# Performance work log

Measured on AMD Instinct MI355X. Metric: run time of the kernel, lower is better.

The kernel has to match this reference:

```python
import jax, jax.numpy as jnp
import numpy as np

# ---- static config (matches init_kwargs) ----
OC, IC, K, S, PAD = 128, 64, 3, 1, 1
M, T, R = 5, 8, 2.5            # ALSH m, table_size, LSH bucket width r
SPAN = K * K * IC              # kernel_span = 576


def setup_inputs() -> dict:
    key = jax.random.key(0)
    k1, k2, k3, k4 = jax.random.split(key, 4)
    # xavier_uniform on the (OC, SPAN) kernel matrix
    bound = float(np.sqrt(6.0 / (OC + SPAN)))
    kernels = jax.random.uniform(k1, (OC, SPAN), minval=-bound, maxval=bound, dtype=jnp.float32)
    a = jax.random.normal(k2, (SPAN + M,), dtype=jnp.float32)          # LSH projection
    b = jax.random.uniform(k3, (), minval=0.0, maxval=R, dtype=jnp.float32)  # LSH offset
    x = jax.random.normal(k4, (16, IC, 56, 56), dtype=jnp.float32)
    return {"x": x, "kernels": kernels, "a": a, "b": b, "mode": 0}


def _im2col(x):
    # [B, SPAN, H2, W2] with feature order (C, kh, kw)
    p = jax.lax.conv_general_dilated_patches(x, (K, K), (S, S), [(PAD, PAD), (PAD, PAD)])
    B, _, H2, W2 = p.shape
    # patch matrix [SPAN, B*H2*W2]
    return p.transpose(1, 0, 2, 3).reshape(SPAN, -1), B, H2, W2


def _bucket(h):
    # floor((h+b)/r); fmod table_size; abs  (matches torch .fmod_ then .abs_)
    return jnp.abs(jnp.fmod(h.astype(jnp.int32), T))


def reference(x, kernels, a, b, mode):
    patch_matr, B, H2, W2 = _im2col(x)            # [SPAN, N], N = B*H2*W2

    # ---- vote: hash every patch column with Q-augmentation (append m halves) ----
    v = a[:SPAN] @ patch_matr + 0.5 * jnp.sum(a[SPAN:])      # [N]
    votes = _bucket(jnp.floor((v + b) / R))
    counts = jnp.zeros((T,), jnp.int32).at[votes].add(1)
    bucket = jnp.argmax(counts)                               # most common bucket

    # ---- hash table: hash each kernel row with P-augmentation (norm powers) ----
    norms2 = jnp.sum(kernels * kernels, axis=1)               # ||k||^2, [OC]
    powers = jnp.stack([norms2 ** (2 ** i) for i in range(M)], axis=1)  # ||k||^{2,4,...,2^M}
    hk = kernels @ a[:SPAN] + powers @ a[SPAN:]               # [OC]
    kidx = _bucket(jnp.floor((hk + b) / R))                   # bucket of each kernel

    # ---- select kernels in the winning bucket; scale by |rows|/OC ----
    mask = (kidx == bucket).astype(x.dtype)                   # [OC]
    cnt = jnp.sum(mask)
    # original gathers the selected rows (variable oc); we scatter back to the
    # full OC channels (zeros for inactive kernels) for static shapes.
    # empty bucket -> dense conv with all kernels, no rescale.
    factor = jnp.where(cnt > 0, mask * (OC / jnp.maximum(cnt, 1.0)), jnp.ones_like(mask))

    out = (kernels * factor[:, None]) @ patch_matr            # [OC, N]
    out = out.reshape(OC, B, H2 * W2).transpose(1, 0, 2)
    return out.reshape(B, OC, H2, W2)
```

## Files before the change

### kernel.cpp

```cpp
#include <hip/hip_runtime.h>
#include <math.h>

#define IC 64
#define OC 128
#define HH 56
#define WW 56
#define BATCH 16
#define HP 58
#define HW (HH*WW)
#define NPIX (BATCH*HW)
#define SPAN 576
#define TSIZE 8
#define VBANDS 28
#define VBLOCKS (BATCH*VBANDS)
#define W2BASE  VBLOCKS
#define BORDBASE (VBLOCKS + OC)
#define NBLK1 (BORDBASE + BATCH)

typedef unsigned short ushort_t;
typedef unsigned int uint_t;
typedef __attribute__((ext_vector_type(8))) __bf16 bf16x8;
typedef __attribute__((ext_vector_type(4))) float f32x4;

__device__ __forceinline__ ushort_t bf16_rne(float f) {
  uint_t u = __builtin_bit_cast(uint_t, f);
  u += 0x7FFFu + ((u >> 16) & 1u);
  return (ushort_t)(u >> 16);
}

__global__ __launch_bounds__(256)
void prep_kernel(const float* __restrict__ x, const float* __restrict__ kernels,
                 const float* __restrict__ a, const float* __restrict__ bptr,
                 ushort_t* __restrict__ xpad, ushort_t* __restrict__ w2,
                 int* __restrict__ rbucket, int* __restrict__ hist_partial) {
  __shared__ float tl[224 * 9];
  __shared__ ushort_t lx[112 * 66];
  __shared__ int hist[TSIZE];
  __shared__ float red0[256], red1[256];
  const int bx = blockIdx.x, t = threadIdx.x;

  if (bx < VBLOCKS) {
    const int b = bx / VBANDS, band = bx % VBANDS;
    const int r0 = band * 2;
    if (t < TSIZE) hist[t] = 0;
    if (t < 224) {
      const int prow = r0 - 1 + t / 56;
      const int col = t % 56;
      const bool inr = ((unsigned)prow < (unsigned)HH);
      const bool mid = (t >= 56 && t < 168);
      const float* xb = x + (size_t)b * IC * HW + (inr ? prow * WW + col : 0);
      ushort_t* lxp = lx + (mid ? (t - 56) : 0) * 66;
      float t9[9] = {0, 0, 0, 0, 0, 0, 0, 0, 0};
      #pragma unroll 8
      for (int c = 0; c < IC; ++c) {
        float xv = inr ? xb[(size_t)c * HW] : 0.0f;
        #pragma unroll
        for (int tap = 0; tap < 9; ++tap) t9[tap] += a[c * 9 + tap] * xv;
        if (mid) lxp[c] = bf16_rne(xv);
      }
      #pragma unroll
      for (int tap = 0; tap < 9; ++tap) tl[t * 9 + tap] = t9[tap];
    }
    __syncthreads();
    if (t < 112) {
      int lr = t / 56, col = t % 56;
      float v = 0.0f;
      #pragma unroll
      for (int kh = 0; kh < 3; ++kh) {
        int gr = r0 + lr - 1 + kh;
        #pragma unroll
        for (int kw = 0; kw < 3; ++kw) {
          int cc = col - 1 + kw;
          if ((unsigned)gr < (unsigned)HH && (unsigned)cc < (unsigned)WW)
            v += tl[((lr + kh) * 56 + cc) * 9 + (kh * 3 + kw)];
        }
      }
      float tail = 0.5f * (a[576] + a[577] + a[578] + a[579] + a[580]);
      int hi = (int)floorf((v + tail + bptr[0]) / 2.5f);
      int r = hi % TSIZE;
      if (r < 0) r = -r;
      atomicAdd(&hist[r], 1);
    }
    {
      const uint_t* lxu = (const uint_t*)lx;
      uint_t* xp = (uint_t*)xpad;
      #pragma unroll
      for (int j = 0; j < 14; ++j) {
        int idx = j * 256 + t;
        int px = idx >> 5, cp = idx & 31;
        int lr = px / 56, c0 = px % 56;
        int y = r0 + 1 + lr, xw = c0 + 1;
        xp[(((size_t)(b * HP + y)) * HP + xw) * 32 + cp] = lxu[px * 33 + cp];
      }
    }
    __syncthreads();
    if (t < TSIZE) hist_partial[bx * TSIZE + t] = hist[t];
  } else if (bx < BORDBASE) {
    const int r = bx - W2BASE;
    const float* row = kernels + (size_t)r * SPAN;
    float d = 0.0f, n2 = 0.0f;
    #pragma unroll
    for (int k0 = 0; k0 < 3; ++k0) {
      int k = k0 * 256 + t;
      if (k < SPAN) { float kv = row[k]; d += kv * a[k]; n2 += kv * kv; }
    }
    red0[t] = d; red1[t] = n2;
    __syncthreads();
    for (int s = 128; s > 0; s >>= 1) {
      if (t < s) { red0[t] += red0[t + s]; red1[t] += red1[t + s]; }
      __syncthreads();
    }
    if (t == 0) {
      float hk = red0[0], p = red1[0];
      #pragma unroll
      for (int i = 0; i < 5; ++i) { hk += p * a[SPAN + i]; p = p * p; }
      int hi = (int)floorf((hk + bptr[0]) / 2.5f);
      int rr = hi % TSIZE;
      if (rr < 0) rr = -rr;
      rbucket[r] = rr;
    }
    #pragma unroll
    for (int j0 = 0; j0 < 3; ++j0) {
      int j = j0 * 256 + t;
      if (j < SPAN) {
        int tap = j >> 6, c = j & 63;
        w2[(size_t)r * SPAN + j] = bf16_rne(row[c * 9 + tap]);
      }
    }
  } else {
    const int ib = bx - BORDBASE;
    uint_t* xp = (uint_t*)xpad + (size_t)ib * HP * HP * 32;
    for (int j = t; j < 7296; j += 256) {
      int px = j >> 5, cp = j & 31;
      int y, xw;
      if (px < 58) { y = 0; xw = px; }
      else if (px < 116) { y = 57; xw = px - 58; }
      else { int k = px - 116; y = 1 + (k >> 1); xw = (k & 1) * 57; }
      xp[((size_t)y * HP + xw) * 32 + cp] = 0;
    }
  }
}

__global__ __launch_bounds__(256, 4)
void gemm_kernel(const ushort_t* __restrict__ w2, const ushort_t* __restrict__ xpad,
                 const int* __restrict__ hist_partial, const int* __restrict__ rbucket,
                 float* __restrict__ out) {
  __shared__ ushort_t As[128 * 64];
  __shared__ ushort_t Bs[64 * 64];
  __shared__ float factor_s[OC];
  __shared__ int counts_s[TSIZE];
  __shared__ int cnt_w[4];
  const int tid = threadIdx.x;
  const int wave = tid >> 6, lane = tid & 63;
  const int n0 = blockIdx.x * 64;
  const int wm = wave * 32;

  const int srow = lane >> 3;
  const int sch = (lane & 7) ^ srow;

  int agbase[4], bgbase[2];
  #pragma unroll
  for (int i = 0; i < 4; ++i) {
    int row = wm + i * 8 + srow;
    agbase[i] = row * SPAN + sch * 8;
  }
  #pragma unroll
  for (int i = 0; i < 2; ++i) {
    int brow = wave * 16 + i * 8 + srow;
    int n = n0 + brow;
    int b = n / HW;
    int rem = n % HW;
    int h = rem / WW, w = rem % WW;
    bgbase[i] = ((b * HP + h) * HP + w) * IC + sch * 8;
  }

  f32x4 acc[2][4] = {};

  for (int tap = 0; tap < 9; ++tap) {
    const int kh = tap / 3, kw = tap % 3;
    const int toffA = tap * 64;
    const int toffB = (kh * HP + kw) * IC;
    __syncthreads();
    #pragma unroll
    for (int i = 0; i < 4; ++i)
      __builtin_amdgcn_global_load_lds(
          (const __attribute__((address_space(1))) void*)(w2 + agbase[i] + toffA),
          (__attribute__((address_space(3))) void*)(As + (wm + i * 8) * 64), 16, 0, 0);
    #pragma unroll
    for (int i = 0; i < 2; ++i)
      __builtin_amdgcn_global_load_lds(
          (const __attribute__((address_space(1))) void*)(xpad + bgbase[i] + toffB),
          (__attribute__((address_space(3))) void*)(Bs + (wave * 16 + i * 8) * 64), 16, 0, 0);
    __syncthreads();
    #pragma unroll
    for (int kk = 0; kk < 2; ++kk) {
      const int jf = kk * 4 + (lane >> 4);
      bf16x8 af[2], bfr[4];
      #pragma unroll
      for (int m = 0; m < 2; ++m) {
        int row = wm + m * 16 + (lane & 15);
        int slot = row * 8 + (jf ^ (row & 7));
        af[m] = *(const bf16x8*)(As + slot * 8);
      }
      #pragma unroll
      for (int n = 0; n < 4; ++n) {
        int col = n * 16 + (lane & 15);
        int slot = col * 8 + (jf ^ (col & 7));
        bfr[n] = *(const bf16x8*)(Bs + slot * 8);
      }
      #pragma unroll
      for (int m = 0; m < 2; ++m)
        #pragma unroll
        for (int n = 0; n < 4; ++n)
          acc[m][n] = __builtin_amdgcn_mfma_f32_16x16x32_bf16(af[m], bfr[n], acc[m][n], 0, 0, 0);
    }
  }

  if (tid < TSIZE) counts_s[tid] = 0;
  __syncthreads();
  {
    int bin = tid >> 5;
    int s = 0;
    for (int k = (tid & 31); k < VBLOCKS; k += 32) s += hist_partial[k * TSIZE + bin];
    atomicAdd(&counts_s[bin], s);
  }
  __syncthreads();
  int best = counts_s[0], bi = 0;
  #pragma unroll
  for (int i = 1; i < TSIZE; ++i) { int c = counts_s[i]; if (c > best) { best = c; bi = i; } }
  int isin = (tid < OC) ? ((rbucket[tid] == bi) ? 1 : 0) : 0;
  unsigned long long bal = __ballot(isin != 0);
  if (lane == 0) cnt_w[wave] = __popcll(bal);
  __syncthreads();
  int cnt = cnt_w[0] + cnt_w[1] + cnt_w[2] + cnt_w[3];
  if (tid < OC)
    factor_s[tid] = (cnt > 0) ? (isin ? 128.0f / (float)cnt : 0.0f) : 1.0f;
  __syncthreads();

  #pragma unroll
  for (int n = 0; n < 4; ++n) {
    int np = n0 + n * 16 + (lane & 15);
    int b = np / HW;
    int rem = np % HW;
    float* obase = out + ((size_t)b * OC) * HW + rem;
    #pragma unroll
    for (int m = 0; m < 2; ++m) {
      int ocb = wm + m * 16 + (lane >> 4) * 4;
      #pragma unroll
      for (int r = 0; r < 4; ++r) {
        obase[(size_t)(ocb + r) * HW] = acc[m][n][r] * factor_s[ocb + r];
      }
    }
  }
}

extern "C" void kernel_launch(void* const* d_in, const int* in_sizes, int n_in,
                              void* d_out, int out_size, void* d_ws, size_t ws_size,
                              hipStream_t stream) {
  (void)in_sizes; (void)n_in; (void)out_size; (void)ws_size;
  const float* x = (const float*)d_in[0];
  const float* kernels = (const float*)d_in[1];
  const float* a = (const float*)d_in[2];
  const float* b = (const float*)d_in[3];
  float* out = (float*)d_out;

  char* ws = (char*)d_ws;
  int* rbucket = (int*)ws;
  int* hist_partial = (int*)(ws + 512);
  ushort_t* w2 = (ushort_t*)(ws + 16384);
  ushort_t* xpad = (ushort_t*)(ws + 16384 + 147456);

  prep_kernel<<<NBLK1, 256, 0, stream>>>(x, kernels, a, b, xpad, w2, rbucket, hist_partial);
  gemm_kernel<<<NPIX / 64, 256, 0, stream>>>(w2, xpad, hist_partial, rbucket, out);
}
```

Baseline: 112.3 us.

## Fuse prep and GEMM kernels into one persistent launch with grid barrier

Result: slower. 402.1 us (+257.9%).

```diff
diff --git a/kernel.cpp b/kernel.cpp
--- a/kernel.cpp
+++ b/kernel.cpp
@@ -15,7 +15,8 @@
 #define VBLOCKS (BATCH*VBANDS)
 #define W2BASE  VBLOCKS
 #define BORDBASE (VBLOCKS + OC)
-#define NBLK1 (BORDBASE + BATCH)
+#define NBLK (NPIX/64)
+#define MAGIC 0x13579BDF
 
 typedef unsigned short ushort_t;
 typedef unsigned int uint_t;
@@ -28,28 +29,46 @@
   return (ushort_t)(u >> 16);
 }
 
-__global__ __launch_bounds__(256)
-void prep_kernel(const float* __restrict__ x, const float* __restrict__ kernels,
-                 const float* __restrict__ a, const float* __restrict__ bptr,
-                 ushort_t* __restrict__ xpad, ushort_t* __restrict__ w2,
-                 int* __restrict__ rbucket, int* __restrict__ hist_partial) {
-  __shared__ float tl[224 * 9];
-  __shared__ ushort_t lx[112 * 66];
-  __shared__ int hist[TSIZE];
-  __shared__ float red0[256], red1[256];
-  const int bx = blockIdx.x, t = threadIdx.x;
+union SMem {
+  struct {
+    ushort_t As[128 * 64];
+    ushort_t Bs[64 * 64];
+    float factor[OC];
+    int counts[TSIZE];
+    int cnt_w[4];
+  } g;
+  struct {
+    float tl[224 * 9];
+    ushort_t lx[112 * 66];
+    int hist[TSIZE];
+  } v;
+  struct {
+    float red0[256];
+    float red1[256];
+  } w;
+};
+
+__global__ __launch_bounds__(256, 4)
+void fused_kernel(const float* __restrict__ x, const float* __restrict__ kernels,
+                  const float* __restrict__ a, const float* __restrict__ bptr,
+                  ushort_t* __restrict__ xpad, ushort_t* __restrict__ w2,
+                  int* __restrict__ rbucket, int* __restrict__ hist_partial,
+                  int* __restrict__ bar, float* __restrict__ out) {
+  __shared__ SMem sm;
+  const int bx = blockIdx.x;
+  const int t = threadIdx.x;
 
   if (bx < VBLOCKS) {
     const int b = bx / VBANDS, band = bx % VBANDS;
     const int r0 = band * 2;
-    if (t < TSIZE) hist[t] = 0;
+    if (t < TSIZE) sm.v.hist[t] = 0;
     if (t < 224) {
       const int prow = r0 - 1 + t / 56;
       const int col = t % 56;
       const bool inr = ((unsigned)prow < (unsigned)HH);
       const bool mid = (t >= 56 && t < 168);
       const float* xb = x + (size_t)b * IC * HW + (inr ? prow * WW + col : 0);
-      ushort_t* lxp = lx + (mid ? (t - 56) : 0) * 66;
+      ushort_t* lxp = sm.v.lx + (mid ? (t - 56) : 0) * 66;
       float t9[9] = {0, 0, 0, 0, 0, 0, 0, 0, 0};
       #pragma unroll 8
       for (int c = 0; c < IC; ++c) {
@@ -59,7 +78,7 @@
         if (mid) lxp[c] = bf16_rne(xv);
       }
       #pragma unroll
-      for (int tap = 0; tap < 9; ++tap) tl[t * 9 + tap] = t9[tap];
+      for (int tap = 0; tap < 9; ++tap) sm.v.tl[t * 9 + tap] = t9[tap];
     }
     __syncthreads();
     if (t < 112) {
@@ -72,17 +91,17 @@
         for (int kw = 0; kw < 3; ++kw) {
           int cc = col - 1 + kw;
           if ((unsigned)gr < (unsigned)HH && (unsigned)cc < (unsigned)WW)
-            v += tl[((lr + kh) * 56 + cc) * 9 + (kh * 3 + kw)];
+            v += sm.v.tl[((lr + kh) * 56 + cc) * 9 + (kh * 3 + kw)];
         }
       }
       float tail = 0.5f * (a[576] + a[577] + a[578] + a[579] + a[580]);
       int hi = (int)floorf((v + tail + bptr[0]) / 2.5f);
       int r = hi % TSIZE;
       if (r < 0) r = -r;
-      atomicAdd(&hist[r], 1);
+      atomicAdd(&sm.v.hist[r], 1);
     }
     {
-      const uint_t* lxu = (const uint_t*)lx;
+      const uint_t* lxu = (const uint_t*)sm.v.lx;
       uint_t* xp = (uint_t*)xpad;
       #pragma unroll
       for (int j = 0; j < 14; ++j) {
@@ -94,7 +113,7 @@
       }
     }
     __syncthreads();
-    if (t < TSIZE) hist_partial[bx * TSIZE + t] = hist[t];
+    if (t < TSIZE) hist_partial[bx * TSIZE + t] = sm.v.hist[t];
   } else if (bx < BORDBASE) {
     const int r = bx - W2BASE;
     const float* row = kernels + (size_t)r * SPAN;
@@ -104,14 +123,14 @@
       int k = k0 * 256 + t;
       if (k < SPAN) { float kv = row[k]; d += kv * a[k]; n2 += kv * kv; }
     }
-    red0[t] = d; red1[t] = n2;
+    sm.w.red0[t] = d; sm.w.red1[t] = n2;
     __syncthreads();
     for (int s = 128; s > 0; s >>= 1) {
-      if (t < s) { red0[t] += red0[t + s]; red1[t] += red1[t + s]; }
+      if (t < s) { sm.w.red0[t] += sm.w.red0[t + s]; sm.w.red1[t] += sm.w.red1[t + s]; }
       __syncthreads();
     }
     if (t == 0) {
-      float hk = red0[0], p = red1[0];
+      float hk = sm.w.red0[0], p = sm.w.red1[0];
       #pragma unroll
       for (int i = 0; i < 5; ++i) { hk += p * a[SPAN + i]; p = p * p; }
       int hi = (int)floorf((hk + bptr[0]) / 2.5f);
@@ -127,7 +146,7 @@
         w2[(size_t)r * SPAN + j] = bf16_rne(row[c * 9 + tap]);
       }
     }
-  } else {
+  } else if (bx < BORDBASE + BATCH) {
     const int ib = bx - BORDBASE;
     uint_t* xp = (uint_t*)xpad + (size_t)ib * HP * HP * 32;
     for (int j = t; j < 7296; j += 256) {
@@ -139,20 +158,35 @@
       xp[((size_t)y * HP + xw) * 32 + cp] = 0;
     }
   }
-}
-
-__global__ __launch_bounds__(256, 4)
-void gemm_kernel(const ushort_t* __restrict__ w2, const ushort_t* __restrict__ xpad,
-                 const int* __restrict__ hist_partial, const int* __restrict__ rbucket,
-                 float* __restrict__ out) {
-  __shared__ ushort_t As[128 * 64];
-  __shared__ ushort_t Bs[64 * 64];
-  __shared__ float factor_s[OC];
-  __shared__ int counts_s[TSIZE];
-  __shared__ int cnt_w[4];
-  const int tid = threadIdx.x;
-  const int wave = tid >> 6, lane = tid & 63;
-  const int n0 = blockIdx.x * 64;
+
+  __syncthreads();
+  if (t == 0) {
+    if (bx == 0) {
+      #pragma unroll
+      for (int i = 0; i < 8; ++i)
+        __hip_atomic_store(&bar[16 + i * 16], 0, __ATOMIC_RELAXED, __HIP_MEMORY_SCOPE_AGENT);
+      __hip_atomic_store(&bar[0], MAGIC, __ATOMIC_RELEASE, __HIP_MEMORY_SCOPE_AGENT);
+    } else {
+      int it = 0;
+      while (__hip_atomic_load(&bar[0], __ATOMIC_ACQUIRE, __HIP_MEMORY_SCOPE_AGENT) != MAGIC
+             && ++it < (1 << 26))
+        __builtin_amdgcn_s_sleep(2);
+    }
+    __hip_atomic_fetch_add(&bar[16 + (bx & 7) * 16], 1, __ATOMIC_ACQ_REL, __HIP_MEMORY_SCOPE_AGENT);
+    int it = 0;
+    for (;;) {
+      int sum = 0;
+      #pragma unroll
+      for (int i = 0; i < 8; ++i)
+        sum += __hip_atomic_load(&bar[16 + i * 16], __ATOMIC_ACQUIRE, __HIP_MEMORY_SCOPE_AGENT);
+      if (sum >= NBLK || ++it >= (1 << 26)) break;
+      __builtin_amdgcn_s_sleep(2);
+    }
+  }
+  __syncthreads();
+
+  const int wave = t >> 6, lane = t & 63;
+  const int n0 = bx * 64;
   const int wm = wave * 32;
 
   const int srow = lane >> 3;
@@ -185,12 +219,12 @@
     for (int i = 0; i < 4; ++i)
       __builtin_amdgcn_global_load_lds(
           (const __attribute__((address_space(1))) void*)(w2 + agbase[i] + toffA),
-          (__attribute__((address_space(3))) void*)(As + (wm + i * 8) * 64), 16, 0, 0);
+          (__attribute__((address_space(3))) void*)(sm.g.As + (wm + i * 8) * 64), 16, 0, 0);
     #pragma unroll
     for (int i = 0; i < 2; ++i)
       __builtin_amdgcn_global_load_lds(
           (const __attribute__((address_space(1))) void*)(xpad + bgbase[i] + toffB),
-          (__attribute__((address_space(3))) void*)(Bs + (wave * 16 + i * 8) * 64), 16, 0, 0);
+          (__attribute__((address_space(3))) void*)(sm.g.Bs + (wave * 16 + i * 8) * 64), 16, 0, 0);
     __syncthreads();
     #pragma unroll
     for (int kk = 0; kk < 2; ++kk) {
@@ -200,13 +234,13 @@
       for (int m = 0; m < 2; ++m) {
         int row = wm + m * 16 + (lane & 15);
         int slot = row * 8 + (jf ^ (row & 7));
-        af[m] = *(const bf16x8*)(As + slot * 8);
+        af[m] = *(const bf16x8*)(sm.g.As + slot * 8);
       }
       #pragma unroll
       for (int n = 0; n < 4; ++n) {
         int col = n * 16 + (lane & 15);
         int slot = col * 8 + (jf ^ (col & 7));
-        bfr[n] = *(const bf16x8*)(Bs + slot * 8);
+        bfr[n] = *(const bf16x8*)(sm.g.Bs + slot * 8);
       }
       #pragma unroll
       for (int m = 0; m < 2; ++m)
@@ -216,25 +250,25 @@
     }
   }
 
-  if (tid < TSIZE) counts_s[tid] = 0;
+  if (t < TSIZE) sm.g.counts[t] = 0;
   __syncthreads();
   {
-    int bin = tid >> 5;
+    int bin = t >> 5;
     int s = 0;
-    for (int k = (tid & 31); k < VBLOCKS; k += 32) s += hist_partial[k * TSIZE + bin];
-    atomicAdd(&counts_s[bin], s);
-  }
-  __syncthreads();
-  int best = counts_s[0], bi = 0;
+    for (int k = (t & 31); k < VBLOCKS; k += 32) s += hist_partial[k * TSIZE + bin];
+    atomicAdd(&sm.g.counts[bin], s);
+  }
+  __syncthreads();
+  int best = sm.g.counts[0], bi = 0;
   #pragma unroll
-  for (int i = 1; i < TSIZE; ++i) { int c = counts_s[i]; if (c > best) { best = c; bi = i; } }
-  int isin = (tid < OC) ? ((rbucket[tid] == bi) ? 1 : 0) : 0;
+  for (int i = 1; i < TSIZE; ++i) { int c = sm.g.counts[i]; if (c > best) { best = c; bi = i; } }
+  int isin = (t < OC) ? ((rbucket[t] == bi) ? 1 : 0) : 0;
   unsigned long long bal = __ballot(isin != 0);
-  if (lane == 0) cnt_w[wave] = __popcll(bal);
-  __syncthreads();
-  int cnt = cnt_w[0] + cnt_w[1] + cnt_w[2] + cnt_w[3];
-  if (tid < OC)
-    factor_s[tid] = (cnt > 0) ? (isin ? 128.0f / (float)cnt : 0.0f) : 1.0f;
+  if (lane == 0) sm.g.cnt_w[wave] = __popcll(bal);
+  __syncthreads();
+  int cnt = sm.g.cnt_w[0] + sm.g.cnt_w[1] + sm.g.cnt_w[2] + sm.g.cnt_w[3];
+  if (t < OC)
+    sm.g.factor[t] = (cnt > 0) ? (isin ? 128.0f / (float)cnt : 0.0f) : 1.0f;
   __syncthreads();
 
   #pragma unroll
@@ -248,7 +282,7 @@
       int ocb = wm + m * 16 + (lane >> 4) * 4;
       #pragma unroll
       for (int r = 0; r < 4; ++r) {
-        obase[(size_t)(ocb + r) * HW] = acc[m][n][r] * factor_s[ocb + r];
+        obase[(size_t)(ocb + r) * HW] = acc[m][n][r] * sm.g.factor[ocb + r];
       }
     }
   }
@@ -267,9 +301,10 @@
   char* ws = (char*)d_ws;
   int* rbucket = (int*)ws;
   int* hist_partial = (int*)(ws + 512);
+  int* bar = (int*)(ws + 15360);
   ushort_t* w2 = (ushort_t*)(ws + 16384);
   ushort_t* xpad = (ushort_t*)(ws + 16384 + 147456);
 
-  prep_kernel<<<NBLK1, 256, 0, stream>>>(x, kernels, a, b, xpad, w2, rbucket, hist_partial);
-  gemm_kernel<<<NPIX / 64, 256, 0, stream>>>(w2, xpad, hist_partial, rbucket, out);
+  fused_kernel<<<NBLK, 256, 0, stream>>>(x, kernels, a, b, xpad, w2,
+                                         rbucket, hist_partial, bar, out);
 }
```

## Pre-swizzle weights into MFMA fragment order for contiguous LDS reads

Applied to the files above, without the earlier changes.

After: 116.0 us. +3.3%, slower.

```diff
diff --git a/kernel.cpp b/kernel.cpp
--- a/kernel.cpp
+++ b/kernel.cpp
@@ -31,7 +31,7 @@
 __global__ __launch_bounds__(256)
 void prep_kernel(const float* __restrict__ x, const float* __restrict__ kernels,
                  const float* __restrict__ a, const float* __restrict__ bptr,
-                 ushort_t* __restrict__ xpad, ushort_t* __restrict__ w2,
+                 ushort_t* __restrict__ xpad, ushort_t* __restrict__ w2m,
                  int* __restrict__ rbucket, int* __restrict__ hist_partial) {
   __shared__ float tl[224 * 9];
   __shared__ ushort_t lx[112 * 66];
@@ -123,8 +123,10 @@
     for (int j0 = 0; j0 < 3; ++j0) {
       int j = j0 * 256 + t;
       if (j < SPAN) {
-        int tap = j >> 6, c = j & 63;
-        w2[(size_t)r * SPAN + j] = bf16_rne(row[c * 9 + tap]);
+        int tap = j / 64, rem = j % 64;
+        int chunk = rem >> 3, c = rem & 7;
+        w2m[(size_t)tap * 8192 + (r >> 4) * 1024 + chunk * 128 + (r & 15) * 8 + c] =
+            bf16_rne(row[rem * 9 + tap]);
       }
     }
   } else {
@@ -142,72 +144,58 @@
 }
 
 __global__ __launch_bounds__(256, 4)
-void gemm_kernel(const ushort_t* __restrict__ w2, const ushort_t* __restrict__ xpad,
+void gemm_kernel(const ushort_t* __restrict__ w2m, const ushort_t* __restrict__ xpad,
                  const int* __restrict__ hist_partial, const int* __restrict__ rbucket,
                  float* __restrict__ out) {
-  __shared__ ushort_t As[128 * 64];
-  __shared__ ushort_t Bs[64 * 64];
+  __shared__ ushort_t As[8192];
+  __shared__ ushort_t Bs[4096];
   __shared__ float factor_s[OC];
   __shared__ int counts_s[TSIZE];
   __shared__ int cnt_w[4];
   const int tid = threadIdx.x;
   const int wave = tid >> 6, lane = tid & 63;
   const int n0 = blockIdx.x * 64;
-  const int wm = wave * 32;
-
-  const int srow = lane >> 3;
-  const int sch = (lane & 7) ^ srow;
-
-  int agbase[4], bgbase[2];
+
+  int aseg[4];
   #pragma unroll
-  for (int i = 0; i < 4; ++i) {
-    int row = wm + i * 8 + srow;
-    agbase[i] = row * SPAN + sch * 8;
-  }
-  #pragma unroll
-  for (int i = 0; i < 2; ++i) {
-    int brow = wave * 16 + i * 8 + srow;
-    int n = n0 + brow;
-    int b = n / HW;
-    int rem = n % HW;
+  for (int i = 0; i < 4; ++i) aseg[i] = (wave * 4 + i) * 512 + lane * 8;
+
+  int bg;
+  {
+    int p = n0 + wave * 16 + (lane & 15);
+    int b = p / HW, rem = p % HW;
     int h = rem / WW, w = rem % WW;
-    bgbase[i] = ((b * HP + h) * HP + w) * IC + sch * 8;
+    bg = ((b * HP + h) * HP + w) * IC + (lane >> 4) * 8;
   }
 
   f32x4 acc[2][4] = {};
 
   for (int tap = 0; tap < 9; ++tap) {
     const int kh = tap / 3, kw = tap % 3;
-    const int toffA = tap * 64;
+    const int toffA = tap * 8192;
     const int toffB = (kh * HP + kw) * IC;
     __syncthreads();
     #pragma unroll
     for (int i = 0; i < 4; ++i)
       __builtin_amdgcn_global_load_lds(
-          (const __attribute__((address_space(1))) void*)(w2 + agbase[i] + toffA),
-          (__attribute__((address_space(3))) void*)(As + (wm + i * 8) * 64), 16, 0, 0);
+          (const __attribute__((address_space(1))) void*)(w2m + toffA + aseg[i]),
+          (__attribute__((address_space(3))) void*)(As + aseg[i]), 16, 0, 0);
     #pragma unroll
     for (int i = 0; i < 2; ++i)
       __builtin_amdgcn_global_load_lds(
-          (const __attribute__((address_space(1))) void*)(xpad + bgbase[i] + toffB),
-          (__attribute__((address_space(3))) void*)(Bs + (wave * 16 + i * 8) * 64), 16, 0, 0);
+          (const __attribute__((address_space(1))) void*)(xpad + bg + toffB + i * 32),
+          (__attribute__((address_space(3))) void*)(Bs + wave * 1024 + i * 512 + lane * 8),
+          16, 0, 0);
     __syncthreads();
     #pragma unroll
     for (int kk = 0; kk < 2; ++kk) {
-      const int jf = kk * 4 + (lane >> 4);
       bf16x8 af[2], bfr[4];
       #pragma unroll
-      for (int m = 0; m < 2; ++m) {
-        int row = wm + m * 16 + (lane & 15);
-        int slot = row * 8 + (jf ^ (row & 7));
-        af[m] = *(const bf16x8*)(As + slot * 8);
-      }
-      #pragma unroll
-      for (int n = 0; n < 4; ++n) {
-        int col = n * 16 + (lane & 15);
-        int slot = col * 8 + (jf ^ (col & 7));
-        bfr[n] = *(const bf16x8*)(Bs + slot * 8);
-      }
+      for (int m = 0; m < 2; ++m)
+        af[m] = *(const bf16x8*)(As + (wave * 2 + m) * 1024 + kk * 512 + lane * 8);
+      #pragma unroll
+      for (int n = 0; n < 4; ++n)
+        bfr[n] = *(const bf16x8*)(Bs + n * 1024 + kk * 512 + lane * 8);
       #pragma unroll
       for (int m = 0; m < 2; ++m)
         #pragma unroll
@@ -237,6 +225,7 @@
     factor_s[tid] = (cnt > 0) ? (isin ? 128.0f / (float)cnt : 0.0f) : 1.0f;
   __syncthreads();
 
+  const int wm = wave * 32;
   #pragma unroll
   for (int n = 0; n < 4; ++n) {
     int np = n0 + n * 16 + (lane & 15);
@@ -267,9 +256,9 @@
   char* ws = (char*)d_ws;
   int* rbucket = (int*)ws;
   int* hist_partial = (int*)(ws + 512);
-  ushort_t* w2 = (ushort_t*)(ws + 16384);
+  ushort_t* w2m = (ushort_t*)(ws + 16384);
   ushort_t* xpad = (ushort_t*)(ws + 16384 + 147456);
 
-  prep_kernel<<<NBLK1, 256, 0, stream>>>(x, kernels, a, b, xpad, w2, rbucket, hist_partial);
-  gemm_kernel<<<NPIX / 64, 256, 0, stream>>>(w2, xpad, hist_partial, rbucket, out);
-}
+  prep_kernel<<<NBLK1, 256, 0, stream>>>(x, kernels, a, b, xpad, w2m, rbucket, hist_partial);
+  gemm_kernel<<<NPIX / 64, 256, 0, stream>>>(w2m, xpad, hist_partial, rbucket, out);
+}
```
